# Optimization experiments

Measured on AMD Instinct MI355X. Metric: run time of the kernel, lower is better.

The kernel has to match this reference:

```python
import jax, jax.numpy as jnp
import numpy as np

N, E, G, ND, H, C, L = 100000, 640000, 1000, 128, 128, 10, 4
ATOMS_PER_GRAPH = 100  # N = G * ATOMS_PER_GRAPH
NEG_SLOPE = 0.01  # nn.LeakyReLU default


def setup_inputs() -> dict:
    key = jax.random.key(0)
    ks = jax.random.split(key, 16)
    s = 0.05
    return {
        "node_attr": jax.random.normal(ks[0], (N, ND), jnp.float32),
        "edge_index": jax.random.randint(ks[1], (2, E), 0, N, jnp.int64),
        "num_atoms": jnp.full((G,), ATOMS_PER_GRAPH, dtype=jnp.int64),
        "enc_W": jax.random.normal(ks[2], (ND, H), jnp.float32) * s,
        "enc_b": jnp.zeros((H,), jnp.float32),
        "gcn_W": jax.random.normal(ks[3], (L, H, H), jnp.float32) * s,
        "gcn_b": jnp.zeros((L, H), jnp.float32),
        "r_W1": jax.random.normal(ks[4], (H, H), jnp.float32) * s,
        "r_b1": jnp.zeros((H,), jnp.float32),
        "r_W2": jax.random.normal(ks[5], (H, H), jnp.float32) * s,
        "r_b2": jnp.zeros((H,), jnp.float32),
        "s_W1": jax.random.normal(ks[6], (H, H), jnp.float32) * s,
        "s_b1": jnp.zeros((H,), jnp.float32),
        "s_W2": jax.random.normal(ks[7], (H, H), jnp.float32) * s,
        "s_b2": jnp.zeros((H,), jnp.float32),
        "fin_W": jax.random.normal(ks[8], (H, C), jnp.float32) * s,
        "fin_b": jnp.zeros((C,), jnp.float32),
    }


def _leaky(x):
    return jnp.where(x > 0, x, NEG_SLOPE * x)


def reference(node_attr, edge_index, num_atoms, enc_W, enc_b, gcn_W, gcn_b,
              r_W1, r_b1, r_W2, r_b2, s_W1, s_b1, s_W2, s_b2, fin_W, fin_b):
    dst, src = edge_index[0], edge_index[1]
    # degree normalization constant across layers: deg(i) = in-edge count, divide by deg+1
    deg = jax.ops.segment_sum(jnp.ones((E,), node_attr.dtype), dst, num_segments=N)
    inv_deg = 1.0 / (deg + 1.0)  # [N]

    x = node_attr @ enc_W + enc_b  # [N, H]
    for l in range(L):
        h = x @ gcn_W[l] + gcn_b[l]
        agg = jax.ops.segment_sum(h[src], dst, num_segments=N)  # scatter_sum over dst
        x = (h + agg) * inv_deg[:, None]

    # GateMLP: ReLuMLP(x) * SigmoidMLP(x)
    r = _leaky(_leaky(x @ r_W1 + r_b1) @ r_W2 + r_b2)
    g = jax.nn.sigmoid(_leaky(x @ s_W1 + s_b1) @ s_W2 + s_b2)
    x = r * g  # [N, H]

    # graph pooling: scatter_mean over graph ids
    graph_mask = jnp.repeat(jnp.arange(G), num_atoms, total_repeat_length=N)
    gsum = jax.ops.segment_sum(x, graph_mask, num_segments=G)
    cnt = jax.ops.segment_sum(jnp.ones((N,), x.dtype), graph_mask, num_segments=G)
    graph_attr = gsum / jnp.maximum(cnt, 1.0)[:, None]  # [G, H]
    return graph_attr @ fin_W + fin_b  # [G, C]
```

## Files before the change

### kernel.cpp

```cpp
#include <hip/hip_runtime.h>
#include <hip/hip_bf16.h>
#include <cstddef>
#include <cstdint>

#define CAP 32
#define LEAK 0.01f

typedef __attribute__((ext_vector_type(8))) short short8v;
typedef __attribute__((ext_vector_type(4))) float float4v;

__device__ __forceinline__ unsigned short f2bf(float f) {
    uint32_t u = __float_as_uint(f);
    uint32_t r = (u + 0x7FFFu + ((u >> 16) & 1u)) >> 16;
    return (unsigned short)r;
}
__device__ __forceinline__ float bf2f(unsigned short s) {
    return __uint_as_float(((uint32_t)s) << 16);
}

__global__ __launch_bounds__(256) void prep(const int* __restrict__ ei, int E_,
                                            int* __restrict__ cnt,
                                            int* __restrict__ bucket,
                                            const float* __restrict__ node_attr,
                                            unsigned short* __restrict__ bx, int Nn,
                                            const float* __restrict__ enc_W,
                                            const float* __restrict__ gcn_W,
                                            const float* __restrict__ rw1,
                                            const float* __restrict__ rw2,
                                            const float* __restrict__ sw1,
                                            const float* __restrict__ sw2,
                                            const float* __restrict__ enc_b,
                                            const float* __restrict__ gcn_b,
                                            const float* __restrict__ rb1,
                                            const float* __restrict__ sb1,
                                            unsigned short* __restrict__ wpack,
                                            float* __restrict__ fold32,
                                            float* __restrict__ fbias,
                                            const int* __restrict__ na,
                                            int* __restrict__ goff, int G_,
                                            int NB_EDGE, int NB_CVT) {
    const int b = blockIdx.x;
    const int tid = threadIdx.x;

    if (b < NB_EDGE) {
        int e = (b * 256 + tid) * 4;
        if (e >= E_) return;
        if (e + 4 <= E_) {
            int4 d4 = *(const int4*)&ei[e];
            int4 s4 = *(const int4*)&ei[(size_t)E_ + e];
            int p0 = atomicAdd(&cnt[d4.x], 1);
            int p1 = atomicAdd(&cnt[d4.y], 1);
            int p2 = atomicAdd(&cnt[d4.z], 1);
            int p3 = atomicAdd(&cnt[d4.w], 1);
            if (p0 < CAP) bucket[(size_t)d4.x * CAP + p0] = s4.x;
            if (p1 < CAP) bucket[(size_t)d4.y * CAP + p1] = s4.y;
            if (p2 < CAP) bucket[(size_t)d4.z * CAP + p2] = s4.z;
            if (p3 < CAP) bucket[(size_t)d4.w * CAP + p3] = s4.w;
        } else {
            for (; e < E_; ++e) {
                int d = ei[e], s = ei[(size_t)E_ + e];
                int p = atomicAdd(&cnt[d], 1);
                if (p < CAP) bucket[(size_t)d * CAP + p] = s;
            }
        }
        return;
    }
    if (b < NB_EDGE + NB_CVT) {
        size_t i8 = ((size_t)(b - NB_EDGE) * 256 + tid) * 8;
        if (i8 < (size_t)Nn * 128) {
            const float* ap = node_attr + i8;
            float4v p = *(const float4v*)ap;
            float4v q = *(const float4v*)(ap + 4);
            short8v v;
            v[0] = (short)f2bf(p[0]); v[1] = (short)f2bf(p[1]);
            v[2] = (short)f2bf(p[2]); v[3] = (short)f2bf(p[3]);
            v[4] = (short)f2bf(q[0]); v[5] = (short)f2bf(q[1]);
            v[6] = (short)f2bf(q[2]); v[7] = (short)f2bf(q[3]);
            *(short8v*)(bx + i8) = v;
        }
        return;
    }
    if (b < NB_EDGE + NB_CVT + 16) {
        int pb = b - (NB_EDGE + NB_CVT);
        int m = (pb < 8) ? 6 : 8;
        int idx = (pb & 7) * 256 + tid;
        const float* W = (m == 6) ? rw2 : sw2;
        int n = idx & 127;
        int fg = (idx >> 7) & 3;
        int kc = idx >> 9;
        short8v v;
#pragma unroll
        for (int j = 0; j < 8; ++j)
            v[j] = (short)f2bf(W[(size_t)(kc * 32 + fg * 8 + j) * 128 + n]);
        *(short8v*)(wpack + (size_t)m * 16384 + (size_t)idx * 8) = v;
        return;
    }
    int fb = b - (NB_EDGE + NB_CVT + 16);
    if (fb < 256) {
        int which = fb >> 6;
        int r = (fb & 63) * 2 + (tid >> 7);
        int n = tid & 127;
        const float* L;
        const float* R;
        switch (which) {
            case 0: L = enc_W;                       R = gcn_W;                 break;
            case 1: L = gcn_W + (size_t)1 * 16384;   R = gcn_W + (size_t)2 * 16384; break;
            case 2: L = gcn_W + (size_t)3 * 16384;   R = rw1;                   break;
            default: L = gcn_W + (size_t)3 * 16384;  R = sw1;                   break;
        }
        float acc = 0.f;
#pragma unroll 8
        for (int k = 0; k < 128; ++k)
            acc = fmaf(L[(size_t)r * 128 + k], R[(size_t)k * 128 + n], acc);
        fold32[(size_t)which * 16384 + (size_t)r * 128 + n] = acc;
        return;
    }
    fb -= 256;
    if (fb == 0) {
        __shared__ float betaL[128];
        if (tid < 128) betaL[tid] = enc_b[tid];
        __syncthreads();
        for (int l = 0; l < 4; ++l) {
            const float* Wl = gcn_W + (size_t)l * 16384;
            float acc = 0.f;
            if (tid < 128) {
                acc = gcn_b[l * 128 + tid];
                for (int k = 0; k < 128; ++k)
                    acc = fmaf(betaL[k], Wl[(size_t)k * 128 + tid], acc);
            }
            __syncthreads();
            if (tid < 128) betaL[tid] = acc;
            __syncthreads();
        }
        if (tid < 128) {
            float a1 = rb1[tid], a2 = sb1[tid];
            for (int k = 0; k < 128; ++k) {
                float bk = betaL[k];
                a1 = fmaf(bk, rw1[(size_t)k * 128 + tid], a1);
                a2 = fmaf(bk, sw1[(size_t)k * 128 + tid], a2);
            }
            fbias[128 + tid] = a1;
            fbias[256 + tid] = a2;
        }
        return;
    }
    if (fb == 1) {
        __shared__ int sh[256];
        int base = tid * 4;
        int v0 = (base + 0 < G_) ? na[base + 0] : 0;
        int v1 = (base + 1 < G_) ? na[base + 1] : 0;
        int v2 = (base + 2 < G_) ? na[base + 2] : 0;
        int v3 = (base + 3 < G_) ? na[base + 3] : 0;
        int s = v0 + v1 + v2 + v3;
        sh[tid] = s;
        __syncthreads();
        for (int ofs = 1; ofs < 256; ofs <<= 1) {
            int u = (tid >= ofs) ? sh[tid - ofs] : 0;
            __syncthreads();
            sh[tid] += u;
            __syncthreads();
        }
        int run = sh[tid] - s;
        if (tid == 0) goff[0] = 0;
        run += v0; if (base + 0 < G_) goff[base + 1] = run;
        run += v1; if (base + 1 < G_) goff[base + 2] = run;
        run += v2; if (base + 2 < G_) goff[base + 3] = run;
        run += v3; if (base + 3 < G_) goff[base + 4] = run;
    }
}

__device__ __forceinline__ void acc8(float a[8], uint4 v, float m) {
    a[0] = fmaf(m, bf2f((unsigned short)(v.x & 0xffff)), a[0]);
    a[1] = fmaf(m, bf2f((unsigned short)(v.x >> 16)), a[1]);
    a[2] = fmaf(m, bf2f((unsigned short)(v.y & 0xffff)), a[2]);
    a[3] = fmaf(m, bf2f((unsigned short)(v.y >> 16)), a[3]);
    a[4] = fmaf(m, bf2f((unsigned short)(v.z & 0xffff)), a[4]);
    a[5] = fmaf(m, bf2f((unsigned short)(v.z >> 16)), a[5]);
    a[6] = fmaf(m, bf2f((unsigned short)(v.w & 0xffff)), a[6]);
    a[7] = fmaf(m, bf2f((unsigned short)(v.w >> 16)), a[7]);
}

__device__ __forceinline__ void issue4(const char* __restrict__ xb, int2 prep_,
                                       int gl, int l16, int Nn, int jb, uint4 V[4]) {
    const int sl = gl + (jb >> 1);
    int s0 = __shfl(prep_.x, sl);
    int s1 = __shfl(prep_.y, sl);
    int s2 = __shfl(prep_.x, sl + 1);
    int s3 = __shfl(prep_.y, sl + 1);
    s0 = min(max(s0, 0), Nn - 1);
    s1 = min(max(s1, 0), Nn - 1);
    s2 = min(max(s2, 0), Nn - 1);
    s3 = min(max(s3, 0), Nn - 1);
    V[0] = *(const uint4*)(xb + (size_t)s0 * 256 + l16 * 16);
    V[1] = *(const uint4*)(xb + (size_t)s1 * 256 + l16 * 16);
    V[2] = *(const uint4*)(xb + (size_t)s2 * 256 + l16 * 16);
    V[3] = *(const uint4*)(xb + (size_t)s3 * 256 + l16 * 16);
}

__device__ __forceinline__ void consume4(float a[8], const uint4 V[4], int jb, int d) {
    acc8(a, V[0], (jb + 0 < d) ? 1.f : 0.f);
    acc8(a, V[1], (jb + 1 < d) ? 1.f : 0.f);
    acc8(a, V[2], (jb + 2 < d) ? 1.f : 0.f);
    acc8(a, V[3], (jb + 3 < d) ? 1.f : 0.f);
}

template <int FM>
__global__ __launch_bounds__(256, 4) void agg_pass(const unsigned short* __restrict__ x,
                                                   const int* __restrict__ bucket,
                                                   const int* __restrict__ cnt,
                                                   unsigned short* __restrict__ xout,
                                                   int Nn, int aggGrid,
                                                   float* __restrict__ fold32,
                                                   unsigned short* __restrict__ wpack) {
    if (FM != 0 && (int)blockIdx.x >= aggGrid) {
        const int tid = threadIdx.x;
        const int e = blockIdx.x - aggGrid;
        if (FM == 1) {
            int r = e * 2 + (tid >> 7), n = tid & 127;
            const float* A = fold32;
            const float* B = fold32 + 16384;
            float acc = 0.f;
#pragma unroll 8
            for (int k = 0; k < 128; ++k)
                acc = fmaf(A[(size_t)r * 128 + k], B[(size_t)k * 128 + n], acc);
            fold32[65536 + (size_t)r * 128 + n] = acc;
        } else {
            int panel = e >> 6;
            int r = (e & 63) * 2 + (tid >> 7), n = tid & 127;
            const float* Ep = fold32 + 65536;
            const float* CD = fold32 + (size_t)(2 + panel) * 16384;
            float acc = 0.f;
#pragma unroll 8
            for (int k = 0; k < 128; ++k)
                acc = fmaf(Ep[(size_t)r * 128 + k], CD[(size_t)k * 128 + n], acc);
            int kc = r >> 5, fg2 = (r >> 3) & 3, j = r & 7;
            wpack[(size_t)(9 + panel) * 16384 +
                  (size_t)(((kc * 4 + fg2) * 128 + n) * 8 + j)] = f2bf(acc);
        }
        return;
    }

    const int tid = threadIdx.x;
    const int lane = tid & 63;
    const int w = tid >> 6;
    const int row0 = blockIdx.x * 64;
    const int l16 = lane & 15;
    const int g = lane >> 4;
    const int gl = lane & 48;
    const char* xb = (const char*)x;

    int cfull = 0;
    if (lane < 16) {
        int gn = row0 + w * 16 + lane;
        if (gn >= Nn) gn = Nn - 1;
        cfull = cnt[gn];
    }
    uint4 own[4];
    int2 pre[4];
#pragma unroll
    for (int p = 0; p < 4; ++p) {
        int gn = row0 + w * 16 + p * 4 + g;
        if (gn >= Nn) gn = Nn - 1;
        own[p] = *(const uint4*)(xb + (size_t)gn * 256 + l16 * 16);
        pre[p] = *(const int2*)&bucket[(size_t)gn * CAP + 2 * l16];
    }

#pragma unroll
    for (int p = 0; p < 4; ++p) {
        const int n = p * 4 + g;
        const int r = w * 16 + n;
        const int dfull = __shfl(cfull, n);
        const float id = 1.0f / (float)(dfull + 1);
        const int d = min(dfull, CAP);

        uint4 VA[4], VB[4];
        issue4(xb, pre[p], gl, l16, Nn, 0, VA);

        float a[8];
        {
            uint4 o = own[p];
            a[0] = bf2f((unsigned short)(o.x & 0xffff));
            a[1] = bf2f((unsigned short)(o.x >> 16));
            a[2] = bf2f((unsigned short)(o.y & 0xffff));
            a[3] = bf2f((unsigned short)(o.y >> 16));
            a[4] = bf2f((unsigned short)(o.z & 0xffff));
            a[5] = bf2f((unsigned short)(o.z >> 16));
            a[6] = bf2f((unsigned short)(o.w & 0xffff));
            a[7] = bf2f((unsigned short)(o.w >> 16));
        }

        int j = 0;
        while (true) {
            if (j + 4 < d) issue4(xb, pre[p], gl, l16, Nn, j + 4, VB);
            consume4(a, VA, j, d);
            j += 4;
            if (j >= d) break;
            if (j + 4 < d) issue4(xb, pre[p], gl, l16, Nn, j + 4, VA);
            consume4(a, VB, j, d);
            j += 4;
            if (j >= d) break;
        }

#pragma unroll
        for (int i = 0; i < 8; ++i) a[i] *= id;
        uint4 o;
        o.x = (uint32_t)f2bf(a[0]) | ((uint32_t)f2bf(a[1]) << 16);
        o.y = (uint32_t)f2bf(a[2]) | ((uint32_t)f2bf(a[3]) << 16);
        o.z = (uint32_t)f2bf(a[4]) | ((uint32_t)f2bf(a[5]) << 16);
        o.w = (uint32_t)f2bf(a[6]) | ((uint32_t)f2bf(a[7]) << 16);
        int node = row0 + r;
        if (node < Nn)
            *(uint4*)((char*)xout + (size_t)node * 256 + l16 * 16) = o;
    }
}

__global__ __launch_bounds__(512, 4) void gate_fused(const unsigned short* __restrict__ x,
                                                     const unsigned short* __restrict__ wpack,
                                                     const float* __restrict__ rb1f,
                                                     const float* __restrict__ rb2,
                                                     const float* __restrict__ sb1f,
                                                     const float* __restrict__ sb2,
                                                     unsigned short* __restrict__ out, int M) {
    __shared__ unsigned short Ws[2 * 128 * 128];
    const int tid = threadIdx.x;
    const int lane = tid & 63;
    const int w = tid >> 6;
    const int l16 = lane & 15;
    const int fg = lane >> 4;
    const int row0 = blockIdx.x * 128 + w * 16;

    int xr = row0 + l16;
    if (xr >= M) xr = M - 1;
    short8v xbf[4];
#pragma unroll
    for (int kc = 0; kc < 4; ++kc)
        xbf[kc] = *(const short8v*)(x + (size_t)xr * 128 + kc * 32 + fg * 8);

    const short8v* WL = (const short8v*)Ws;
    uint32_t upR[8][2], upS[8][2];

    union { uint32_t u[4]; short8v v; } cvt;

#define STAGE2(mi0, mi1)                                                      \
    {                                                                         \
        const short8v* s0 = (const short8v*)(wpack + (size_t)(mi0) * 16384);  \
        const short8v* s1 = (const short8v*)(wpack + (size_t)(mi1) * 16384);  \
        short8v* dst = (short8v*)Ws;                                          \
        _Pragma("unroll") for (int i = 0; i < 4; ++i)                         \
            dst[i * 512 + tid] = s0[i * 512 + tid];                          \
        _Pragma("unroll") for (int i = 0; i < 4; ++i)                         \
            dst[2048 + i * 512 + tid] = s1[i * 512 + tid];                    \
    }

#define PASS1(OFS, BIAS, UP)                                                  \
    _Pragma("unroll") for (int nt = 0; nt < 8; ++nt) {                        \
        float4v acc = (float4v){0.f, 0.f, 0.f, 0.f};                          \
        _Pragma("unroll") for (int kc = 0; kc < 4; ++kc)                      \
            acc = __builtin_amdgcn_mfma_f32_16x16x32_bf16(                    \
                WL[(OFS) + (kc * 4 + fg) * 128 + nt * 16 + l16], xbf[kc], acc, 0, 0, 0); \
        _Pragma("unroll") for (int q = 0; q < 4; ++q) {                       \
            float v = acc[q] + (BIAS)[nt * 16 + fg * 4 + q];                  \
            acc[q] = v > 0.f ? v : LEAK * v;                                  \
        }                                                                     \
        UP[nt][0] = (uint32_t)f2bf(acc[0]) | ((uint32_t)f2bf(acc[1]) << 16);  \
        UP[nt][1] = (uint32_t)f2bf(acc[2]) | ((uint32_t)f2bf(acc[3]) << 16);  \
    }

#define MKUF(UP, UF)                                                          \
    _Pragma("unroll") for (int kc = 0; kc < 4; ++kc) {                        \
        uint32_t pr0, pr1, pr2, pr3;                                          \
        {                                                                     \
            int srcl = (((2 * fg + 0) & 3) << 4) + l16;                       \
            uint32_t lo = __shfl((int)UP[2 * kc][0], srcl);                   \
            uint32_t hi = __shfl((int)UP[2 * kc + 1][0], srcl);               \
            pr0 = (fg & 2) ? hi : lo;                                         \
            lo = __shfl((int)UP[2 * kc][1], srcl);                            \
            hi = __shfl((int)UP[2 * kc + 1][1], srcl);                        \
            pr1 = (fg & 2) ? hi : lo;                                         \
        }                                                                     \
        {                                                                     \
            int srcl = (((2 * fg + 1) & 3) << 4) + l16;                       \
            uint32_t lo = __shfl((int)UP[2 * kc][0], srcl);                   \
            uint32_t hi = __shfl((int)UP[2 * kc + 1][0], srcl);               \
            pr2 = (fg & 2) ? hi : lo;                                         \
            lo = __shfl((int)UP[2 * kc][1], srcl);                            \
            hi = __shfl((int)UP[2 * kc + 1][1], srcl);                        \
            pr3 = (fg & 2) ? hi : lo;                                         \
        }                                                                     \
        cvt.u[0] = pr0; cvt.u[1] = pr1; cvt.u[2] = pr2; cvt.u[3] = pr3;       \
        UF[kc] = cvt.v;                                                       \
    }

    STAGE2(9, 10);
    __syncthreads();
    PASS1(0, rb1f, upR);
    PASS1(2048, sb1f, upS);
    __syncthreads();

    STAGE2(6, 8);
    __syncthreads();

    short8v uf[4];
    MKUF(upR, uf);
    float4v rf[8];
#pragma unroll
    for (int t2 = 0; t2 < 8; ++t2) {
        float4v acc = (float4v){0.f, 0.f, 0.f, 0.f};
#pragma unroll
        for (int kc = 0; kc < 4; ++kc)
            acc = __builtin_amdgcn_mfma_f32_16x16x32_bf16(
                uf[kc], WL[(kc * 4 + fg) * 128 + t2 * 16 + l16], acc, 0, 0, 0);
        const float bv = rb2[t2 * 16 + l16];
#pragma unroll
        for (int q = 0; q < 4; ++q) {
            float v = acc[q] + bv;
            rf[t2][q] = v > 0.f ? v : LEAK * v;
        }
    }

    MKUF(upS, uf);
#pragma unroll
    for (int t2 = 0; t2 < 8; ++t2) {
        float4v acc = (float4v){0.f, 0.f, 0.f, 0.f};
#pragma unroll
        for (int kc = 0; kc < 4; ++kc)
            acc = __builtin_amdgcn_mfma_f32_16x16x32_bf16(
                uf[kc], WL[2048 + (kc * 4 + fg) * 128 + t2 * 16 + l16], acc, 0, 0, 0);
        const float bv = sb2[t2 * 16 + l16];
#pragma unroll
        for (int q = 0; q < 4; ++q) {
            int row = row0 + fg * 4 + q;
            if (row < M) {
                float gg = 1.f / (1.f + __expf(-(acc[q] + bv)));
                out[(size_t)row * 128 + t2 * 16 + l16] = f2bf(gg * rf[t2][q]);
            }
        }
    }
#undef STAGE2
#undef PASS1
#undef MKUF
}

__global__ void pool(const unsigned short* __restrict__ x, const int* __restrict__ goff,
                     float* __restrict__ gattr, int G_) {
    int g = blockIdx.x * 2 + (threadIdx.x >> 7);
    if (g >= G_) return;
    int d = threadIdx.x & 127;
    int a0 = goff[g], a1 = goff[g + 1];
    float s0 = 0.f, s1 = 0.f, s2 = 0.f, s3 = 0.f;
    int a = a0;
    for (; a + 4 <= a1; a += 4) {
        s0 += bf2f(__builtin_nontemporal_load(&x[(size_t)(a + 0) * 128 + d]));
        s1 += bf2f(__builtin_nontemporal_load(&x[(size_t)(a + 1) * 128 + d]));
        s2 += bf2f(__builtin_nontemporal_load(&x[(size_t)(a + 2) * 128 + d]));
        s3 += bf2f(__builtin_nontemporal_load(&x[(size_t)(a + 3) * 128 + d]));
    }
    for (; a < a1; ++a) s0 += bf2f(__builtin_nontemporal_load(&x[(size_t)a * 128 + d]));
    float s = (s0 + s1) + (s2 + s3);
    float c = (float)max(a1 - a0, 1);
    gattr[(size_t)g * 128 + d] = s / c;
}

__global__ void final_gemm(const float* __restrict__ gattr, const float* __restrict__ fW,
                           const float* __restrict__ fb, float* __restrict__ out,
                           int G_, int C_) {
    int i = blockIdx.x * 256 + threadIdx.x;
    if (i >= G_ * C_) return;
    int g = i / C_, c = i % C_;
    const float* row = gattr + (size_t)g * 128;
    float s = fb[c];
    for (int k = 0; k < 128; ++k) s = fmaf(row[k], fW[k * C_ + c], s);
    out[i] = s;
}

extern "C" void kernel_launch(void* const* d_in, const int* in_sizes, int n_in,
                              void* d_out, int out_size, void* d_ws, size_t ws_size,
                              hipStream_t stream) {
    const float* node_attr = (const float*)d_in[0];
    const int* edge_index  = (const int*)d_in[1];
    const int* num_atoms   = (const int*)d_in[2];
    const float* enc_W = (const float*)d_in[3];
    const float* enc_b = (const float*)d_in[4];
    const float* gcn_W = (const float*)d_in[5];
    const float* gcn_b = (const float*)d_in[6];
    const float* r_W1 = (const float*)d_in[7];
    const float* r_b1 = (const float*)d_in[8];
    const float* r_W2 = (const float*)d_in[9];
    const float* r_b2 = (const float*)d_in[10];
    const float* s_W1 = (const float*)d_in[11];
    const float* s_b1 = (const float*)d_in[12];
    const float* s_W2 = (const float*)d_in[13];
    const float* s_b2 = (const float*)d_in[14];
    const float* fin_W = (const float*)d_in[15];
    const float* fin_b = (const float*)d_in[16];
    float* out = (float*)d_out;

    const int N_ = in_sizes[0] / 128;
    const int E_ = in_sizes[1] / 2;
    const int G_ = in_sizes[2];
    const int C_ = in_sizes[16];

    size_t off = 0;
    auto alloc = [&](size_t bytes) -> void* {
        void* p = (char*)d_ws + off;
        off += (bytes + 255) & ~(size_t)255;
        return p;
    };
    unsigned short* bx = (unsigned short*)alloc((size_t)N_ * 128 * 2);
    unsigned short* bh = (unsigned short*)alloc((size_t)N_ * 128 * 2);
    int* bucket = (int*)alloc((size_t)N_ * CAP * 4);
    int* cnt    = (int*)alloc((size_t)N_ * 4);
    unsigned short* wpack = (unsigned short*)alloc((size_t)11 * 16384 * 2);
    float* fold32 = (float*)alloc((size_t)5 * 16384 * 4);
    float* fbias = (float*)alloc((size_t)3 * 128 * 4);
    int* goff   = (int*)alloc((size_t)(G_ + 1) * 4);
    float* gattr = (float*)alloc((size_t)G_ * 128 * 4);
    (void)ws_size; (void)n_in; (void)out_size;

    const int agg_grid = (N_ + 63) / 64;
    const int NB_EDGE = (E_ / 4 + 255) / 256;
    const int NB_CVT = (N_ * 16 + 255) / 256;
    const int NB_PREP = NB_EDGE + NB_CVT + 16 + 256 + 2;

    hipMemsetAsync(cnt, 0, (size_t)N_ * 4, stream);
    prep<<<NB_PREP, 256, 0, stream>>>(edge_index, E_, cnt, bucket,
                                      node_attr, bx, N_,
                                      enc_W, gcn_W, r_W1, r_W2, s_W1, s_W2,
                                      enc_b, gcn_b, r_b1, s_b1,
                                      wpack, fold32, fbias, num_atoms, goff, G_,
                                      NB_EDGE, NB_CVT);

    agg_pass<1><<<agg_grid + 64, 256, 0, stream>>>(bx, bucket, cnt, bh, N_,
                                                   agg_grid, fold32, wpack);
    agg_pass<2><<<agg_grid + 128, 256, 0, stream>>>(bh, bucket, cnt, bx, N_,
                                                    agg_grid, fold32, wpack);
    agg_pass<0><<<agg_grid, 256, 0, stream>>>(bx, bucket, cnt, bh, N_,
                                              agg_grid, fold32, wpack);
    agg_pass<0><<<agg_grid, 256, 0, stream>>>(bh, bucket, cnt, bx, N_,
                                              agg_grid, fold32, wpack);

    gate_fused<<<(N_ + 127) / 128, 512, 0, stream>>>(bx, wpack, fbias + 128, r_b2,
                                                     fbias + 256, s_b2, bh, N_);

    pool<<<(G_ + 1) / 2, 256, 0, stream>>>(bh, goff, gattr, G_);
    final_gemm<<<(G_ * C_ + 255) / 256, 256, 0, stream>>>(gattr, fin_W, fin_b, out, G_, C_);
}
```

Baseline: 247.1 us.

## Fold final linear layer into gate kernel before pooling, and widen edge bucketing

The gate kernel now projects each node's gated features through fin_W (a per-node 128→10 dot product with shuffle reductions), so only a 10-wide fp32 row per node is written instead of a 128-wide bf16 row. Because the mean and the linear map commute, pooling then averages these 10-wide rows and adds the bias, which removes the separate pool and final_gemm kernels and most of the intermediate traffic. Separately, each thread in the edge-bucketing prep phase now handles 8 edges instead of 4. The tradeoff is extra shuffles and global fin_W loads inside the gate kernel, plus a different floating-point summation order.

New measurement: 249.2 us. No clear change (+0.9%).

```diff
diff --git a/kernel.cpp b/kernel.cpp
--- a/kernel.cpp
+++ b/kernel.cpp
@@ -43,19 +43,29 @@
     const int tid = threadIdx.x;
 
     if (b < NB_EDGE) {
-        int e = (b * 256 + tid) * 4;
+        int e = (b * 256 + tid) * 8;
         if (e >= E_) return;
-        if (e + 4 <= E_) {
-            int4 d4 = *(const int4*)&ei[e];
-            int4 s4 = *(const int4*)&ei[(size_t)E_ + e];
-            int p0 = atomicAdd(&cnt[d4.x], 1);
-            int p1 = atomicAdd(&cnt[d4.y], 1);
-            int p2 = atomicAdd(&cnt[d4.z], 1);
-            int p3 = atomicAdd(&cnt[d4.w], 1);
-            if (p0 < CAP) bucket[(size_t)d4.x * CAP + p0] = s4.x;
-            if (p1 < CAP) bucket[(size_t)d4.y * CAP + p1] = s4.y;
-            if (p2 < CAP) bucket[(size_t)d4.z * CAP + p2] = s4.z;
-            if (p3 < CAP) bucket[(size_t)d4.w * CAP + p3] = s4.w;
+        if (e + 8 <= E_) {
+            int4 da = *(const int4*)&ei[e];
+            int4 db = *(const int4*)&ei[e + 4];
+            int4 sa = *(const int4*)&ei[(size_t)E_ + e];
+            int4 sb = *(const int4*)&ei[(size_t)E_ + e + 4];
+            int p0 = atomicAdd(&cnt[da.x], 1);
+            int p1 = atomicAdd(&cnt[da.y], 1);
+            int p2 = atomicAdd(&cnt[da.z], 1);
+            int p3 = atomicAdd(&cnt[da.w], 1);
+            int p4 = atomicAdd(&cnt[db.x], 1);
+            int p5 = atomicAdd(&cnt[db.y], 1);
+            int p6 = atomicAdd(&cnt[db.z], 1);
+            int p7 = atomicAdd(&cnt[db.w], 1);
+            if (p0 < CAP) bucket[(size_t)da.x * CAP + p0] = sa.x;
+            if (p1 < CAP) bucket[(size_t)da.y * CAP + p1] = sa.y;
+            if (p2 < CAP) bucket[(size_t)da.z * CAP + p2] = sa.z;
+            if (p3 < CAP) bucket[(size_t)da.w * CAP + p3] = sa.w;
+            if (p4 < CAP) bucket[(size_t)db.x * CAP + p4] = sb.x;
+            if (p5 < CAP) bucket[(size_t)db.y * CAP + p5] = sb.y;
+            if (p6 < CAP) bucket[(size_t)db.z * CAP + p6] = sb.z;
+            if (p7 < CAP) bucket[(size_t)db.w * CAP + p7] = sb.w;
         } else {
             for (; e < E_; ++e) {
                 int d = ei[e], s = ei[(size_t)E_ + e];
@@ -320,7 +330,8 @@
                                                      const float* __restrict__ rb2,
                                                      const float* __restrict__ sb1f,
                                                      const float* __restrict__ sb2,
-                                                     unsigned short* __restrict__ out, int M) {
+                                                     const float* __restrict__ finW,
+                                                     float* __restrict__ y, int M) {
     __shared__ unsigned short Ws[2 * 128 * 128];
     const int tid = threadIdx.x;
     const int lane = tid & 63;
@@ -429,10 +440,30 @@
         const float bv = sb2[t2 * 16 + l16];
 #pragma unroll
         for (int q = 0; q < 4; ++q) {
-            int row = row0 + fg * 4 + q;
-            if (row < M) {
-                float gg = 1.f / (1.f + __expf(-(acc[q] + bv)));
-                out[(size_t)row * 128 + t2 * 16 + l16] = f2bf(gg * rf[t2][q]);
+            float gg = 1.f / (1.f + __expf(-(acc[q] + bv)));
+            rf[t2][q] *= gg;
+        }
+    }
+
+#pragma unroll 1
+    for (int c = 0; c < 10; ++c) {
+        float fw[8];
+#pragma unroll
+        for (int t2 = 0; t2 < 8; ++t2)
+            fw[t2] = finW[(size_t)(t2 * 16 + l16) * 10 + c];
+#pragma unroll
+        for (int q = 0; q < 4; ++q) {
+            float p = 0.f;
+#pragma unroll
+            for (int t2 = 0; t2 < 8; ++t2)
+                p = fmaf(rf[t2][q], fw[t2], p);
+            p += __shfl_xor(p, 1);
+            p += __shfl_xor(p, 2);
+            p += __shfl_xor(p, 4);
+            p += __shfl_xor(p, 8);
+            if (l16 == 0) {
+                int row = row0 + fg * 4 + q;
+                if (row < M) y[(size_t)row * 10 + c] = p;
             }
         }
     }
@@ -441,36 +472,25 @@
 #undef MKUF
 }
 
-__global__ void pool(const unsigned short* __restrict__ x, const int* __restrict__ goff,
-                     float* __restrict__ gattr, int G_) {
-    int g = blockIdx.x * 2 + (threadIdx.x >> 7);
-    if (g >= G_) return;
-    int d = threadIdx.x & 127;
+__global__ void pool10(const float* __restrict__ y, const int* __restrict__ goff,
+                       const float* __restrict__ fb, float* __restrict__ out, int G_) {
+    __shared__ float sh[16][16];
+    int g = blockIdx.x;
+    int c = threadIdx.x & 15;
+    int rg = threadIdx.x >> 4;
     int a0 = goff[g], a1 = goff[g + 1];
-    float s0 = 0.f, s1 = 0.f, s2 = 0.f, s3 = 0.f;
-    int a = a0;
-    for (; a + 4 <= a1; a += 4) {
-        s0 += bf2f(__builtin_nontemporal_load(&x[(size_t)(a + 0) * 128 + d]));
-        s1 += bf2f(__builtin_nontemporal_load(&x[(size_t)(a + 1) * 128 + d]));
-        s2 += bf2f(__builtin_nontemporal_load(&x[(size_t)(a + 2) * 128 + d]));
-        s3 += bf2f(__builtin_nontemporal_load(&x[(size_t)(a + 3) * 128 + d]));
-    }
-    for (; a < a1; ++a) s0 += bf2f(__builtin_nontemporal_load(&x[(size_t)a * 128 + d]));
-    float s = (s0 + s1) + (s2 + s3);
-    float c = (float)max(a1 - a0, 1);
-    gattr[(size_t)g * 128 + d] = s / c;
-}
-
-__global__ void final_gemm(const float* __restrict__ gattr, const float* __restrict__ fW,
-                           const float* __restrict__ fb, float* __restrict__ out,
-                           int G_, int C_) {
-    int i = blockIdx.x * 256 + threadIdx.x;
-    if (i >= G_ * C_) return;
-    int g = i / C_, c = i % C_;
-    const float* row = gattr + (size_t)g * 128;
-    float s = fb[c];
-    for (int k = 0; k < 128; ++k) s = fmaf(row[k], fW[k * C_ + c], s);
-    out[i] = s;
+    float s = 0.f;
+    if (c < 10)
+        for (int r = a0 + rg; r < a1; r += 16)
+            s += y[(size_t)r * 10 + c];
+    sh[rg][c] = s;
+    __syncthreads();
+    if (rg == 0 && c < 10) {
+        float tot = 0.f;
+#pragma unroll
+        for (int i = 0; i < 16; ++i) tot += sh[i][c];
+        out[(size_t)g * 10 + c] = tot / (float)max(a1 - a0, 1) + fb[c];
+    }
 }
 
 extern "C" void kernel_launch(void* const* d_in, const int* in_sizes, int n_in,
@@ -498,7 +518,6 @@
     const int N_ = in_sizes[0] / 128;
     const int E_ = in_sizes[1] / 2;
     const int G_ = in_sizes[2];
-    const int C_ = in_sizes[16];
 
     size_t off = 0;
     auto alloc = [&](size_t bytes) -> void* {
@@ -513,12 +532,12 @@
     unsigned short* wpack = (unsigned short*)alloc((size_t)11 * 16384 * 2);
     float* fold32 = (float*)alloc((size_t)5 * 16384 * 4);
     float* fbias = (float*)alloc((size_t)3 * 128 * 4);
+    float* ybuf = (float*)alloc((size_t)N_ * 10 * 4);
     int* goff   = (int*)alloc((size_t)(G_ + 1) * 4);
-    float* gattr = (float*)alloc((size_t)G_ * 128 * 4);
     (void)ws_size; (void)n_in; (void)out_size;
 
     const int agg_grid = (N_ + 63) / 64;
-    const int NB_EDGE = (E_ / 4 + 255) / 256;
+    const int NB_EDGE = (E_ / 8 + 255) / 256;
     const int NB_CVT = (N_ * 16 + 255) / 256;
     const int NB_PREP = NB_EDGE + NB_CVT + 16 + 256 + 2;
 
@@ -540,8 +559,7 @@
                                               agg_grid, fold32, wpack);
 
     gate_fused<<<(N_ + 127) / 128, 512, 0, stream>>>(bx, wpack, fbias + 128, r_b2,
-                                                     fbias + 256, s_b2, bh, N_);
-
-    pool<<<(G_ + 1) / 2, 256, 0, stream>>>(bh, goff, gattr, G_);
-    final_gemm<<<(G_ * C_ + 255) / 256, 256, 0, stream>>>(gattr, fin_W, fin_b, out, G_, C_);
-}
+                                                     fbias + 256, s_b2, fin_W, ybuf, N_);
+
+    pool10<<<G_, 256, 0, stream>>>(ybuf, goff, fin_b, out, G_);
+}
```
